# Optimization experiments

Hardware: AMD Instinct MI355X
Metric: run time of the kernel (lower is better)

## Reference

```python
import jax, jax.numpy as jnp
import numpy as np

NUM_NEURONS = 10000
D = 784
BATCH = 4096


def setup_inputs() -> dict:
    key = jax.random.key(0)
    kx, kw = jax.random.split(key)
    x = jax.random.normal(kx, (BATCH, D), dtype=jnp.float32)
    weights = jax.random.normal(kw, (NUM_NEURONS, D), dtype=jnp.float32)
    return {"x": x, "weights": weights}


def reference(x, weights):
    # SOM BMU lookup: squared distances between each input row and every
    # codebook row, argmin over the codebook, gather the winning neuron.
    # Use |a|^2 + |b|^2 - 2ab to avoid the (B, N, D) broadcast intermediate.
    x = x.reshape(-1, D)  # (B, D)
    x_sq = jnp.sum(x * x, axis=1, keepdims=True)          # (B, 1)
    w_sq = jnp.sum(weights * weights, axis=1)             # (N,)
    cross = x @ weights.T                                 # (B, N) GEMM
    distances = x_sq + w_sq[None, :] - 2.0 * cross        # (B, N)
    bmu_indices = jnp.argmin(distances, axis=1)           # (B,)
    bmu = jnp.take(weights, bmu_indices, axis=0)          # (B, D)
    return bmu
```

## Files before the change

### kernel.cpp

```cpp
#include <hip/hip_runtime.h>
#include <math.h>

#define BATCH 4096
#define D 784
#define N 10000

#define KP 800
#define NPAD 10112
#define NCHUNK 79
#define BM 128
#define BN 128
#define BK 32
#define KPL 40
#define MARGIN 3.0f

typedef __attribute__((ext_vector_type(8))) short bh8;
typedef __attribute__((ext_vector_type(4))) float fx4;

static __device__ __forceinline__ unsigned short f2bf(float f) {
    unsigned u = __float_as_uint(f);
    unsigned r = u + 0x7fffu + ((u >> 16) & 1u);
    return (unsigned short)(r >> 16);
}

static __device__ __forceinline__ void top2_insert(float w, int j, float& v0, int& i0,
                                                   float& v1, int& i1) {
    if (w < v0 || (w == v0 && j < i0)) { v1 = v0; i1 = i0; v0 = w; i0 = j; }
    else if (w < v1 || (w == v1 && j < i1)) { v1 = w; i1 = j; }
}

__global__ __launch_bounds__(256) void convert_x_kernel(const float* __restrict__ x,
                                                        unsigned short* __restrict__ xh) {
    int row = blockIdx.x;
    const float4* xr = (const float4*)(x + (size_t)row * D);
    unsigned short* dst = xh + (size_t)row * KP;
    for (int i = threadIdx.x; i < KP / 4; i += 256) {
        int k = i * 4;
        uint2 o;
        if (k < D) {
            float4 v = xr[i];
            o.x = (unsigned)f2bf(v.x) | ((unsigned)f2bf(v.y) << 16);
            o.y = (unsigned)f2bf(v.z) | ((unsigned)f2bf(v.w) << 16);
        } else { o.x = 0u; o.y = 0u; }
        *(uint2*)(dst + k) = o;
    }
}

__global__ __launch_bounds__(256) void convert_w_kernel(const float* __restrict__ w,
                                                        unsigned short* __restrict__ wh,
                                                        float* __restrict__ wsq) {
    int row = blockIdx.x;
    unsigned short* dst = wh + (size_t)row * KP;
    float s = 0.f;
    if (row < N) {
        const float4* wr = (const float4*)(w + (size_t)row * D);
        for (int i = threadIdx.x; i < KP / 4; i += 256) {
            int k = i * 4;
            uint2 o;
            if (k < D) {
                float4 v = wr[i];
                s += v.x * v.x + v.y * v.y + v.z * v.z + v.w * v.w;
                o.x = (unsigned)f2bf(v.x) | ((unsigned)f2bf(v.y) << 16);
                o.y = (unsigned)f2bf(v.z) | ((unsigned)f2bf(v.w) << 16);
            } else { o.x = 0u; o.y = 0u; }
            *(uint2*)(dst + k) = o;
        }
    } else {
        for (int i = threadIdx.x; i < KP / 4; i += 256) {
            uint2 o; o.x = 0u; o.y = 0u;
            *(uint2*)(dst + i * 4) = o;
        }
    }
    __shared__ float sred[4];
    #pragma unroll
    for (int off = 32; off; off >>= 1) s += __shfl_down(s, off);
    if ((threadIdx.x & 63) == 0) sred[threadIdx.x >> 6] = s;
    __syncthreads();
    if (threadIdx.x == 0) {
        float t = sred[0] + sred[1] + sred[2] + sred[3];
        wsq[row] = (row < N) ? t : INFINITY;
    }
}

__global__ __launch_bounds__(256) void dist_mfma_kernel(
    const unsigned short* __restrict__ xh, const unsigned short* __restrict__ wh,
    const float* __restrict__ wsq, float4* __restrict__ partial) {
    __shared__ __align__(16) unsigned short as_[BM][KPL];
    __shared__ __align__(16) unsigned short bs_[BN][KPL];
    __shared__ float4 red[BM][2];

    int tid = threadIdx.x;
    int lane = tid & 63;
    int wid = tid >> 6;
    int waveM = (wid >> 1) * 64;
    int waveN = (wid & 1) * 64;
    int rowBase = blockIdx.y * BM;
    int colBase = blockIdx.x * BN;

    fx4 acc[4][4];
    #pragma unroll
    for (int m = 0; m < 4; m++)
        #pragma unroll
        for (int n = 0; n < 4; n++) acc[m][n] = (fx4)0.f;

    int lrow = tid >> 1;
    int lseg = tid & 1;
    const unsigned short* xsrc = xh + (size_t)(rowBase + lrow) * KP + lseg * 16;
    const unsigned short* wsrc = wh + (size_t)(colBase + lrow) * KP + lseg * 16;

    for (int k0 = 0; k0 < KP; k0 += BK) {
        uint4 xa = *(const uint4*)(xsrc + k0);
        uint4 xb = *(const uint4*)(xsrc + k0 + 8);
        uint4 wa = *(const uint4*)(wsrc + k0);
        uint4 wb = *(const uint4*)(wsrc + k0 + 8);
        __syncthreads();
        *(uint4*)&as_[lrow][lseg * 16]     = xa;
        *(uint4*)&as_[lrow][lseg * 16 + 8] = xb;
        *(uint4*)&bs_[lrow][lseg * 16]     = wa;
        *(uint4*)&bs_[lrow][lseg * 16 + 8] = wb;
        __syncthreads();

        bh8 af[4], bf[4];
        #pragma unroll
        for (int m = 0; m < 4; m++)
            af[m] = *(const bh8*)&as_[waveM + m * 16 + (lane & 15)][(lane >> 4) * 8];
        #pragma unroll
        for (int n = 0; n < 4; n++)
            bf[n] = *(const bh8*)&bs_[waveN + n * 16 + (lane & 15)][(lane >> 4) * 8];
        #pragma unroll
        for (int m = 0; m < 4; m++)
            #pragma unroll
            for (int n = 0; n < 4; n++)
                acc[m][n] = __builtin_amdgcn_mfma_f32_16x16x32_bf16(af[m], bf[n],
                                                                    acc[m][n], 0, 0, 0);
    }

    float wq[4];
    #pragma unroll
    for (int n = 0; n < 4; n++)
        wq[n] = wsq[colBase + waveN + n * 16 + (lane & 15)];

    int h = lane >> 4;
    #pragma unroll
    for (int m = 0; m < 4; m++) {
        #pragma unroll
        for (int r = 0; r < 4; r++) {
            int row_local = waveM + m * 16 + h * 4 + r;
            float v0 = INFINITY, v1 = INFINITY;
            int i0 = 0x7fffffff, i1 = 0x7fffffff;
            #pragma unroll
            for (int n = 0; n < 4; n++) {
                float dv = wq[n] - 2.f * acc[m][n][r];
                int ci = colBase + waveN + n * 16 + (lane & 15);
                top2_insert(dv, ci, v0, i0, v1, i1);
            }
            #pragma unroll
            for (int mask = 1; mask < 16; mask <<= 1) {
                float w0 = __shfl_xor(v0, mask); int j0 = __shfl_xor(i0, mask);
                float w1 = __shfl_xor(v1, mask); int j1 = __shfl_xor(i1, mask);
                top2_insert(w0, j0, v0, i0, v1, i1);
                top2_insert(w1, j1, v0, i0, v1, i1);
            }
            if ((lane & 15) == 0)
                red[row_local][wid & 1] =
                    make_float4(v0, __int_as_float(i0), v1, __int_as_float(i1));
        }
    }
    __syncthreads();
    if (tid < BM) {
        float4 pa = red[tid][0], pb = red[tid][1];
        float v0 = pa.x, v1 = pa.z;
        int i0 = __float_as_int(pa.y), i1 = __float_as_int(pa.w);
        top2_insert(pb.x, __float_as_int(pb.y), v0, i0, v1, i1);
        top2_insert(pb.z, __float_as_int(pb.w), v0, i0, v1, i1);
        partial[(size_t)(rowBase + tid) * NCHUNK + blockIdx.x] =
            make_float4(v0, __int_as_float(i0), v1, __int_as_float(i1));
    }
}

__global__ __launch_bounds__(256) void rescore_kernel(const float* __restrict__ x,
                                                      const float* __restrict__ w,
                                                      const float4* __restrict__ partial,
                                                      float* __restrict__ out) {
    int wid = threadIdx.x >> 6, lane = threadIdx.x & 63;
    int row = blockIdx.x * 4 + wid;
    __shared__ int s_cnt[4];
    __shared__ int s_cand[4][64];

    const float4* part = partial + (size_t)row * NCHUNK;

    float bv = INFINITY;
    for (int c = lane; c < NCHUNK; c += 64) bv = fminf(bv, part[c].x);
    #pragma unroll
    for (int mask = 1; mask < 64; mask <<= 1) bv = fminf(bv, __shfl_xor(bv, mask));
    float thr = bv + MARGIN;

    if (lane == 0) s_cnt[wid] = 0;
    __syncthreads();
    for (int c = lane; c < NCHUNK; c += 64) {
        float4 p = part[c];
        if (p.x <= thr) {
            int pos = atomicAdd(&s_cnt[wid], 1);
            if (pos < 64) s_cand[wid][pos] = __float_as_int(p.y);
        }
        if (p.z <= thr) {
            int pos = atomicAdd(&s_cnt[wid], 1);
            if (pos < 64) s_cand[wid][pos] = __float_as_int(p.w);
        }
    }
    __syncthreads();
    int cnt = s_cnt[wid]; if (cnt > 64) cnt = 64;

    double bd = INFINITY; int bi = 0x7fffffff;
    for (int c = 0; c < cnt; c++) {
        int idx = s_cand[wid][c];
        const float* wr = w + (size_t)idx * D;
        const float* xr = x + (size_t)row * D;
        double s = 0.0;
        for (int d = lane; d < D; d += 64) {
            double wv = (double)wr[d];
            s += wv * (wv - 2.0 * (double)xr[d]);
        }
        #pragma unroll
        for (int mask = 1; mask < 64; mask <<= 1) s += __shfl_xor(s, mask);
        if (s < bd || (s == bd && idx < bi)) { bd = s; bi = idx; }
    }

    const float4* src = (const float4*)(w + (size_t)bi * D);
    float4* dst = (float4*)(out + (size_t)row * D);
    for (int i = lane; i < D / 4; i += 64) dst[i] = src[i];
}

#define FTM 64
#define FTN 128
#define FKC 16
#define FNCHUNK ((N + FTN - 1) / FTN)

__global__ __launch_bounds__(256) void wsq_kernel(const float* __restrict__ w,
                                                  float* __restrict__ wsq) {
    int row = blockIdx.x * 4 + (threadIdx.x >> 6);
    int lane = threadIdx.x & 63;
    if (row >= N) return;
    const float4* wr4 = (const float4*)(w + (size_t)row * D);
    float s = 0.f;
    for (int i = lane; i < D / 4; i += 64) {
        float4 v = wr4[i];
        s += v.x * v.x + v.y * v.y + v.z * v.z + v.w * v.w;
    }
    #pragma unroll
    for (int off = 32; off; off >>= 1) s += __shfl_down(s, off);
    if (lane == 0) wsq[row] = s;
}

__global__ __launch_bounds__(256) void dist_argmin_kernel(
    const float* __restrict__ x, const float* __restrict__ w,
    const float* __restrict__ wsq, float2* __restrict__ partial) {
    __shared__ float xs[FKC][68];
    __shared__ float wsh[FKC][132];
    int tid = threadIdx.x;
    int rowBase = blockIdx.y * FTM;
    int colBase = blockIdx.x * FTN;
    int tr = tid >> 4, tc = tid & 15;
    float acc[4][8];
    #pragma unroll
    for (int i = 0; i < 4; i++)
        #pragma unroll
        for (int j = 0; j < 8; j++) acc[i][j] = 0.f;
    int xrow = tid >> 2, xseg = tid & 3;
    for (int k0 = 0; k0 < D; k0 += FKC) {
        float4 xv = *(const float4*)&x[(size_t)(rowBase + xrow) * D + k0 + xseg * 4];
        int c0 = colBase + xrow, c1 = colBase + xrow + 64;
        float4 wv0 = (c0 < N) ? *(const float4*)&w[(size_t)c0 * D + k0 + xseg * 4]
                              : make_float4(0.f, 0.f, 0.f, 0.f);
        float4 wv1 = (c1 < N) ? *(const float4*)&w[(size_t)c1 * D + k0 + xseg * 4]
                              : make_float4(0.f, 0.f, 0.f, 0.f);
        __syncthreads();
        xs[xseg * 4 + 0][xrow] = xv.x; xs[xseg * 4 + 1][xrow] = xv.y;
        xs[xseg * 4 + 2][xrow] = xv.z; xs[xseg * 4 + 3][xrow] = xv.w;
        wsh[xseg * 4 + 0][xrow] = wv0.x; wsh[xseg * 4 + 1][xrow] = wv0.y;
        wsh[xseg * 4 + 2][xrow] = wv0.z; wsh[xseg * 4 + 3][xrow] = wv0.w;
        wsh[xseg * 4 + 0][xrow + 64] = wv1.x; wsh[xseg * 4 + 1][xrow + 64] = wv1.y;
        wsh[xseg * 4 + 2][xrow + 64] = wv1.z; wsh[xseg * 4 + 3][xrow + 64] = wv1.w;
        __syncthreads();
        #pragma unroll
        for (int k = 0; k < FKC; k++) {
            float4 a = *(const float4*)&xs[k][tr * 4];
            float4 b0 = *(const float4*)&wsh[k][tc * 8];
            float4 b1 = *(const float4*)&wsh[k][tc * 8 + 4];
            float xa[4] = {a.x, a.y, a.z, a.w};
            float wb[8] = {b0.x, b0.y, b0.z, b0.w, b1.x, b1.y, b1.z, b1.w};
            #pragma unroll
            for (int i = 0; i < 4; i++)
                #pragma unroll
                for (int j = 0; j < 8; j++) acc[i][j] = fmaf(xa[i], wb[j], acc[i][j]);
        }
    }
    float bestv[4]; int besti[4];
    #pragma unroll
    for (int i = 0; i < 4; i++) { bestv[i] = INFINITY; besti[i] = 0x7fffffff; }
    #pragma unroll
    for (int j = 0; j < 8; j++) {
        int c = colBase + tc * 8 + j;
        float wqv = (c < N) ? wsq[c] : INFINITY;
        #pragma unroll
        for (int i = 0; i < 4; i++) {
            float dv = wqv - 2.f * acc[i][j];
            if (dv < bestv[i] || (dv == bestv[i] && c < besti[i])) { bestv[i] = dv; besti[i] = c; }
        }
    }
    #pragma unroll
    for (int off = 1; off < 16; off <<= 1) {
        #pragma unroll
        for (int i = 0; i < 4; i++) {
            float ov = __shfl_xor(bestv[i], off);
            int oi = __shfl_xor(besti[i], off);
            if (ov < bestv[i] || (ov == bestv[i] && oi < besti[i])) { bestv[i] = ov; besti[i] = oi; }
        }
    }
    if (tc == 0)
        #pragma unroll
        for (int i = 0; i < 4; i++)
            partial[(size_t)(rowBase + tr * 4 + i) * FNCHUNK + blockIdx.x] =
                make_float2(bestv[i], __int_as_float(besti[i]));
}

__global__ __launch_bounds__(256) void reduce_gather_kernel(
    const float2* __restrict__ partial, const float* __restrict__ w,
    float* __restrict__ out) {
    int row = blockIdx.x, tid = threadIdx.x;
    __shared__ int s_idx;
    if (tid < 64) {
        float bv2 = INFINITY; int bi2 = 0x7fffffff;
        for (int c = tid; c < FNCHUNK; c += 64) {
            float2 p = partial[(size_t)row * FNCHUNK + c];
            int pi = __float_as_int(p.y);
            if (p.x < bv2 || (p.x == bv2 && pi < bi2)) { bv2 = p.x; bi2 = pi; }
        }
        #pragma unroll
        for (int off = 32; off; off >>= 1) {
            float ov = __shfl_down(bv2, off);
            int oi = __shfl_down(bi2, off);
            if (ov < bv2 || (ov == bv2 && oi < bi2)) { bv2 = ov; bi2 = oi; }
        }
        if (tid == 0) s_idx = bi2;
    }
    __syncthreads();
    int idx = s_idx;
    const float4* src = (const float4*)&w[(size_t)idx * D];
    float4* dst = (float4*)&out[(size_t)row * D];
    for (int i = tid; i < D / 4; i += 256) dst[i] = src[i];
}

extern "C" void kernel_launch(void* const* d_in, const int* in_sizes, int n_in,
                              void* d_out, int out_size, void* d_ws, size_t ws_size,
                              hipStream_t stream) {
    const float* x = (const float*)d_in[0];
    const float* w = (const float*)d_in[1];
    float* out = (float*)d_out;

    const size_t off_xh = 0;
    const size_t off_wh = off_xh + (size_t)BATCH * KP * 2;
    const size_t off_wsq = off_wh + (size_t)NPAD * KP * 2;
    const size_t off_part = off_wsq + (size_t)NPAD * 4 + 3648;
    const size_t need = off_part + (size_t)BATCH * NCHUNK * 16;

    if (ws_size >= need) {
        unsigned short* xh = (unsigned short*)((char*)d_ws + off_xh);
        unsigned short* wh = (unsigned short*)((char*)d_ws + off_wh);
        float* wsq = (float*)((char*)d_ws + off_wsq);
        float4* partial = (float4*)((char*)d_ws + off_part);

        hipLaunchKernelGGL(convert_x_kernel, dim3(BATCH), dim3(256), 0, stream, x, xh);
        hipLaunchKernelGGL(convert_w_kernel, dim3(NPAD), dim3(256), 0, stream, w, wh, wsq);
        hipLaunchKernelGGL(dist_mfma_kernel, dim3(NCHUNK, BATCH / BM), dim3(256), 0,
                           stream, xh, wh, wsq, partial);
        hipLaunchKernelGGL(rescore_kernel, dim3(BATCH / 4), dim3(256), 0, stream,
                           x, w, partial, out);
    } else {
        float* wsq = (float*)d_ws;
        float2* partial = (float2*)((char*)d_ws + 65536);
        hipLaunchKernelGGL(wsq_kernel, dim3((N + 3) / 4), dim3(256), 0, stream, w, wsq);
        hipLaunchKernelGGL(dist_argmin_kernel, dim3(FNCHUNK, BATCH / FTM), dim3(256), 0,
                           stream, x, w, wsq, partial);
        hipLaunchKernelGGL(reduce_gather_kernel, dim3(BATCH), dim3(256), 0, stream,
                           partial, w, out);
    }
}
```

Before: 526.2 us.

## Double-buffer MFMA GEMM with direct global-to-LDS loads and multi-chunk blocks

Restructures the bf16 MFMA distance kernel. Tiles are loaded straight into double-buffered, XOR-swizzled LDS with global_load_lds, so the copy overlaps compute and there are fewer barriers per k-step. Each block now walks four column chunks and keeps running top-2 state in registers, which cuts partial outputs and cross-lane reductions. Blocks are remapped for L2 locality, and the fallback path is removed. The cost is higher register pressure from the 16-row top-2 state and a hard dependence on the workspace being large enough.

```diff
diff --git a/kernel.cpp b/kernel.cpp
--- a/kernel.cpp
+++ b/kernel.cpp
@@ -6,16 +6,20 @@
 #define N 10000
 
 #define KP 800
-#define NPAD 10112
-#define NCHUNK 79
+#define BK 32
+#define KT (KP / BK)
 #define BM 128
 #define BN 128
-#define BK 32
-#define KPL 40
+#define CPB 4
+#define GX 20
+#define NG GX
+#define NPAD (GX * CPB * BN)
 #define MARGIN 3.0f
 
 typedef __attribute__((ext_vector_type(8))) short bh8;
 typedef __attribute__((ext_vector_type(4))) float fx4;
+typedef const __attribute__((address_space(1))) void CGV;
+typedef __attribute__((address_space(3))) void LDSV;
 
 static __device__ __forceinline__ unsigned short f2bf(float f) {
     unsigned u = __float_as_uint(f);
@@ -82,88 +86,145 @@
     }
 }
 
-__global__ __launch_bounds__(256) void dist_mfma_kernel(
+__global__ __launch_bounds__(256, 2) void dist_mfma_kernel(
     const unsigned short* __restrict__ xh, const unsigned short* __restrict__ wh,
     const float* __restrict__ wsq, float4* __restrict__ partial) {
-    __shared__ __align__(16) unsigned short as_[BM][KPL];
-    __shared__ __align__(16) unsigned short bs_[BN][KPL];
+    __shared__ __align__(16) unsigned short As[2][BM * BK];
+    __shared__ __align__(16) unsigned short Bs[2][BN * BK];
     __shared__ float4 red[BM][2];
 
-    int tid = threadIdx.x;
-    int lane = tid & 63;
-    int wid = tid >> 6;
-    int waveM = (wid >> 1) * 64;
-    int waveN = (wid & 1) * 64;
-    int rowBase = blockIdx.y * BM;
-    int colBase = blockIdx.x * BN;
-
-    fx4 acc[4][4];
-    #pragma unroll
-    for (int m = 0; m < 4; m++)
-        #pragma unroll
-        for (int n = 0; n < 4; n++) acc[m][n] = (fx4)0.f;
-
-    int lrow = tid >> 1;
-    int lseg = tid & 1;
-    const unsigned short* xsrc = xh + (size_t)(rowBase + lrow) * KP + lseg * 16;
-    const unsigned short* wsrc = wh + (size_t)(colBase + lrow) * KP + lseg * 16;
-
-    for (int k0 = 0; k0 < KP; k0 += BK) {
-        uint4 xa = *(const uint4*)(xsrc + k0);
-        uint4 xb = *(const uint4*)(xsrc + k0 + 8);
-        uint4 wa = *(const uint4*)(wsrc + k0);
-        uint4 wb = *(const uint4*)(wsrc + k0 + 8);
-        __syncthreads();
-        *(uint4*)&as_[lrow][lseg * 16]     = xa;
-        *(uint4*)&as_[lrow][lseg * 16 + 8] = xb;
-        *(uint4*)&bs_[lrow][lseg * 16]     = wa;
-        *(uint4*)&bs_[lrow][lseg * 16 + 8] = wb;
-        __syncthreads();
-
-        bh8 af[4], bf[4];
-        #pragma unroll
-        for (int m = 0; m < 4; m++)
-            af[m] = *(const bh8*)&as_[waveM + m * 16 + (lane & 15)][(lane >> 4) * 8];
-        #pragma unroll
-        for (int n = 0; n < 4; n++)
-            bf[n] = *(const bh8*)&bs_[waveN + n * 16 + (lane & 15)][(lane >> 4) * 8];
+    const int tid = threadIdx.x;
+    const int lane = tid & 63;
+    const int wid = tid >> 6;
+    const int waveM = (wid >> 1) * 64;
+    const int waveN = (wid & 1) * 64;
+
+    const int L = blockIdx.x + GX * blockIdx.y;
+    const int G = (L & 7) * 80 + (L >> 3);
+    const int bx = G >> 5;
+    const int by = G & 31;
+    const int rowBase = by * BM;
+    const int colBase0 = bx * (CPB * BN);
+
+    const int rr = tid >> 2;
+    const int csw = (tid & 3) ^ ((rr >> 1) & 3);
+    const unsigned short* aSrc0 = xh + (size_t)(rowBase + rr) * KP + csw * 8;
+    const unsigned short* aSrc1 = aSrc0 + (size_t)64 * KP;
+
+    char* ldsA0 = (char*)&As[0][0] + wid * 1024;
+    char* ldsA1 = (char*)&As[1][0] + wid * 1024;
+    char* ldsB0 = (char*)&Bs[0][0] + wid * 1024;
+    char* ldsB1 = (char*)&Bs[1][0] + wid * 1024;
+
+    int offA[4], offB[4];
+    #pragma unroll
+    for (int m = 0; m < 4; m++) {
+        int r = waveM + m * 16 + (lane & 15);
+        offA[m] = r * BK + (((lane >> 4) ^ ((r >> 1) & 3)) << 3);
+    }
+    #pragma unroll
+    for (int n = 0; n < 4; n++) {
+        int r = waveN + n * 16 + (lane & 15);
+        offB[n] = r * BK + (((lane >> 4) ^ ((r >> 1) & 3)) << 3);
+    }
+
+    float V0[16], V1[16];
+    int I0[16], I1[16];
+    #pragma unroll
+    for (int q = 0; q < 16; q++) {
+        V0[q] = INFINITY; V1[q] = INFINITY;
+        I0[q] = 0x7fffffff; I1[q] = 0x7fffffff;
+    }
+
+#define STAGE(nb, k0)                                                                  \
+    do {                                                                               \
+        __builtin_amdgcn_global_load_lds((CGV*)(aSrc0 + (k0)), (LDSV*)(ldsA##nb), 16, 0, 0);        \
+        __builtin_amdgcn_global_load_lds((CGV*)(aSrc1 + (k0)), (LDSV*)(ldsA##nb + 4096), 16, 0, 0); \
+        __builtin_amdgcn_global_load_lds((CGV*)(bSrc0 + (k0)), (LDSV*)(ldsB##nb), 16, 0, 0);        \
+        __builtin_amdgcn_global_load_lds((CGV*)(bSrc1 + (k0)), (LDSV*)(ldsB##nb + 4096), 16, 0, 0); \
+    } while (0)
+
+#define COMPUTE(nb)                                                                    \
+    do {                                                                               \
+        bh8 af[4], bf[4];                                                              \
+        _Pragma("unroll")                                                              \
+        for (int m = 0; m < 4; m++) af[m] = *(const bh8*)&As[nb][offA[m]];             \
+        _Pragma("unroll")                                                              \
+        for (int n = 0; n < 4; n++) bf[n] = *(const bh8*)&Bs[nb][offB[n]];             \
+        _Pragma("unroll")                                                              \
+        for (int m = 0; m < 4; m++)                                                    \
+            _Pragma("unroll")                                                          \
+            for (int n = 0; n < 4; n++)                                                \
+                acc[m][n] = __builtin_amdgcn_mfma_f32_16x16x32_bf16(af[m], bf[n],      \
+                                                                    acc[m][n], 0, 0, 0); \
+    } while (0)
+
+#define VM0 asm volatile("s_waitcnt vmcnt(0)" ::: "memory")
+#define BARR __builtin_amdgcn_s_barrier()
+
+    #pragma unroll 1
+    for (int c = 0; c < CPB; ++c) {
+        const int colBase = colBase0 + c * BN;
+        const unsigned short* bSrc0 = wh + (size_t)(colBase + rr) * KP + csw * 8;
+        const unsigned short* bSrc1 = bSrc0 + (size_t)64 * KP;
+
+        fx4 acc[4][4];
         #pragma unroll
         for (int m = 0; m < 4; m++)
             #pragma unroll
-            for (int n = 0; n < 4; n++)
-                acc[m][n] = __builtin_amdgcn_mfma_f32_16x16x32_bf16(af[m], bf[n],
-                                                                    acc[m][n], 0, 0, 0);
-    }
-
-    float wq[4];
-    #pragma unroll
-    for (int n = 0; n < 4; n++)
-        wq[n] = wsq[colBase + waveN + n * 16 + (lane & 15)];
-
-    int h = lane >> 4;
-    #pragma unroll
-    for (int m = 0; m < 4; m++) {
+            for (int n = 0; n < 4; n++) acc[m][n] = (fx4)0.f;
+
+        STAGE(0, 0);
+        VM0; BARR;
+        #pragma unroll 1
+        for (int t = 0; t < KT - 1; t += 2) {
+            STAGE(1, (t + 1) * BK);
+            COMPUTE(0);
+            VM0; BARR;
+            STAGE(0, (t + 2) * BK);
+            COMPUTE(1);
+            VM0; BARR;
+        }
+        COMPUTE(0);
+
+        const int cb = colBase + waveN + (lane & 15);
         #pragma unroll
-        for (int r = 0; r < 4; r++) {
-            int row_local = waveM + m * 16 + h * 4 + r;
-            float v0 = INFINITY, v1 = INFINITY;
-            int i0 = 0x7fffffff, i1 = 0x7fffffff;
+        for (int n = 0; n < 4; n++) {
+            const float wq = wsq[cb + n * 16];
+            const int ci = cb + n * 16;
             #pragma unroll
-            for (int n = 0; n < 4; n++) {
-                float dv = wq[n] - 2.f * acc[m][n][r];
-                int ci = colBase + waveN + n * 16 + (lane & 15);
-                top2_insert(dv, ci, v0, i0, v1, i1);
-            }
-            #pragma unroll
-            for (int mask = 1; mask < 16; mask <<= 1) {
-                float w0 = __shfl_xor(v0, mask); int j0 = __shfl_xor(i0, mask);
-                float w1 = __shfl_xor(v1, mask); int j1 = __shfl_xor(i1, mask);
-                top2_insert(w0, j0, v0, i0, v1, i1);
-                top2_insert(w1, j1, v0, i0, v1, i1);
-            }
-            if ((lane & 15) == 0)
-                red[row_local][wid & 1] =
-                    make_float4(v0, __int_as_float(i0), v1, __int_as_float(i1));
+            for (int m = 0; m < 4; m++)
+                #pragma unroll
+                for (int r = 0; r < 4; r++) {
+                    float dv = wq - 2.f * acc[m][n][r];
+                    top2_insert(dv, ci, V0[m * 4 + r], I0[m * 4 + r],
+                                V1[m * 4 + r], I1[m * 4 + r]);
+                }
+        }
+        __syncthreads();
+    }
+
+#undef STAGE
+#undef COMPUTE
+#undef VM0
+#undef BARR
+
+    #pragma unroll
+    for (int q = 0; q < 16; q++) {
+        float v0 = V0[q], v1 = V1[q];
+        int i0 = I0[q], i1 = I1[q];
+        #pragma unroll
+        for (int mask = 1; mask < 16; mask <<= 1) {
+            float w0 = __shfl_xor(v0, mask); int j0 = __shfl_xor(i0, mask);
+            float w1 = __shfl_xor(v1, mask); int j1 = __shfl_xor(i1, mask);
+            top2_insert(w0, j0, v0, i0, v1, i1);
+            top2_insert(w1, j1, v0, i0, v1, i1);
+        }
+        if ((lane & 15) == 0) {
+            int m = q >> 2, r = q & 3;
+            int row_local = waveM + m * 16 + (lane >> 4) * 4 + r;
+            red[row_local][wid & 1] =
+                make_float4(v0, __int_as_float(i0), v1, __int_as_float(i1));
         }
     }
     __syncthreads();
@@ -173,7 +234,7 @@
         int i0 = __float_as_int(pa.y), i1 = __float_as_int(pa.w);
         top2_insert(pb.x, __float_as_int(pb.y), v0, i0, v1, i1);
         top2_insert(pb.z, __float_as_int(pb.w), v0, i0, v1, i1);
-        partial[(size_t)(rowBase + tid) * NCHUNK + blockIdx.x] =
+        partial[(size_t)(rowBase + tid) * NG + bx] =
             make_float4(v0, __int_as_float(i0), v1, __int_as_float(i1));
     }
 }
@@ -187,17 +248,17 @@
     __shared__ int s_cnt[4];
     __shared__ int s_cand[4][64];
 
-    const float4* part = partial + (size_t)row * NCHUNK;
+    const float4* part = partial + (size_t)row * NG;
 
     float bv = INFINITY;
-    for (int c = lane; c < NCHUNK; c += 64) bv = fminf(bv, part[c].x);
+    for (int c = lane; c < NG; c += 64) bv = fminf(bv, part[c].x);
     #pragma unroll
     for (int mask = 1; mask < 64; mask <<= 1) bv = fminf(bv, __shfl_xor(bv, mask));
     float thr = bv + MARGIN;
 
     if (lane == 0) s_cnt[wid] = 0;
     __syncthreads();
-    for (int c = lane; c < NCHUNK; c += 64) {
+    for (int c = lane; c < NG; c += 64) {
         float4 p = part[c];
         if (p.x <= thr) {
             int pos = atomicAdd(&s_cnt[wid], 1);
@@ -231,126 +292,6 @@
     for (int i = lane; i < D / 4; i += 64) dst[i] = src[i];
 }
 
-#define FTM 64
-#define FTN 128
-#define FKC 16
-#define FNCHUNK ((N + FTN - 1) / FTN)
-
-__global__ __launch_bounds__(256) void wsq_kernel(const float* __restrict__ w,
-                                                  float* __restrict__ wsq) {
-    int row = blockIdx.x * 4 + (threadIdx.x >> 6);
-    int lane = threadIdx.x & 63;
-    if (row >= N) return;
-    const float4* wr4 = (const float4*)(w + (size_t)row * D);
-    float s = 0.f;
-    for (int i = lane; i < D / 4; i += 64) {
-        float4 v = wr4[i];
-        s += v.x * v.x + v.y * v.y + v.z * v.z + v.w * v.w;
-    }
-    #pragma unroll
-    for (int off = 32; off; off >>= 1) s += __shfl_down(s, off);
-    if (lane == 0) wsq[row] = s;
-}
-
-__global__ __launch_bounds__(256) void dist_argmin_kernel(
-    const float* __restrict__ x, const float* __restrict__ w,
-    const float* __restrict__ wsq, float2* __restrict__ partial) {
-    __shared__ float xs[FKC][68];
-    __shared__ float wsh[FKC][132];
-    int tid = threadIdx.x;
-    int rowBase = blockIdx.y * FTM;
-    int colBase = blockIdx.x * FTN;
-    int tr = tid >> 4, tc = tid & 15;
-    float acc[4][8];
-    #pragma unroll
-    for (int i = 0; i < 4; i++)
-        #pragma unroll
-        for (int j = 0; j < 8; j++) acc[i][j] = 0.f;
-    int xrow = tid >> 2, xseg = tid & 3;
-    for (int k0 = 0; k0 < D; k0 += FKC) {
-        float4 xv = *(const float4*)&x[(size_t)(rowBase + xrow) * D + k0 + xseg * 4];
-        int c0 = colBase + xrow, c1 = colBase + xrow + 64;
-        float4 wv0 = (c0 < N) ? *(const float4*)&w[(size_t)c0 * D + k0 + xseg * 4]
-                              : make_float4(0.f, 0.f, 0.f, 0.f);
-        float4 wv1 = (c1 < N) ? *(const float4*)&w[(size_t)c1 * D + k0 + xseg * 4]
-                              : make_float4(0.f, 0.f, 0.f, 0.f);
-        __syncthreads();
-        xs[xseg * 4 + 0][xrow] = xv.x; xs[xseg * 4 + 1][xrow] = xv.y;
-        xs[xseg * 4 + 2][xrow] = xv.z; xs[xseg * 4 + 3][xrow] = xv.w;
-        wsh[xseg * 4 + 0][xrow] = wv0.x; wsh[xseg * 4 + 1][xrow] = wv0.y;
-        wsh[xseg * 4 + 2][xrow] = wv0.z; wsh[xseg * 4 + 3][xrow] = wv0.w;
-        wsh[xseg * 4 + 0][xrow + 64] = wv1.x; wsh[xseg * 4 + 1][xrow + 64] = wv1.y;
-        wsh[xseg * 4 + 2][xrow + 64] = wv1.z; wsh[xseg * 4 + 3][xrow + 64] = wv1.w;
-        __syncthreads();
-        #pragma unroll
-        for (int k = 0; k < FKC; k++) {
-            float4 a = *(const float4*)&xs[k][tr * 4];
-            float4 b0 = *(const float4*)&wsh[k][tc * 8];
-            float4 b1 = *(const float4*)&wsh[k][tc * 8 + 4];
-            float xa[4] = {a.x, a.y, a.z, a.w};
-            float wb[8] = {b0.x, b0.y, b0.z, b0.w, b1.x, b1.y, b1.z, b1.w};
-            #pragma unroll
-            for (int i = 0; i < 4; i++)
-                #pragma unroll
-                for (int j = 0; j < 8; j++) acc[i][j] = fmaf(xa[i], wb[j], acc[i][j]);
-        }
-    }
-    float bestv[4]; int besti[4];
-    #pragma unroll
-    for (int i = 0; i < 4; i++) { bestv[i] = INFINITY; besti[i] = 0x7fffffff; }
-    #pragma unroll
-    for (int j = 0; j < 8; j++) {
-        int c = colBase + tc * 8 + j;
-        float wqv = (c < N) ? wsq[c] : INFINITY;
-        #pragma unroll
-        for (int i = 0; i < 4; i++) {
-            float dv = wqv - 2.f * acc[i][j];
-            if (dv < bestv[i] || (dv == bestv[i] && c < besti[i])) { bestv[i] = dv; besti[i] = c; }
-        }
-    }
-    #pragma unroll
-    for (int off = 1; off < 16; off <<= 1) {
-        #pragma unroll
-        for (int i = 0; i < 4; i++) {
-            float ov = __shfl_xor(bestv[i], off);
-            int oi = __shfl_xor(besti[i], off);
-            if (ov < bestv[i] || (ov == bestv[i] && oi < besti[i])) { bestv[i] = ov; besti[i] = oi; }
-        }
-    }
-    if (tc == 0)
-        #pragma unroll
-        for (int i = 0; i < 4; i++)
-            partial[(size_t)(rowBase + tr * 4 + i) * FNCHUNK + blockIdx.x] =
-                make_float2(bestv[i], __int_as_float(besti[i]));
-}
-
-__global__ __launch_bounds__(256) void reduce_gather_kernel(
-    const float2* __restrict__ partial, const float* __restrict__ w,
-    float* __restrict__ out) {
-    int row = blockIdx.x, tid = threadIdx.x;
-    __shared__ int s_idx;
-    if (tid < 64) {
-        float bv2 = INFINITY; int bi2 = 0x7fffffff;
-        for (int c = tid; c < FNCHUNK; c += 64) {
-            float2 p = partial[(size_t)row * FNCHUNK + c];
-            int pi = __float_as_int(p.y);
-            if (p.x < bv2 || (p.x == bv2 && pi < bi2)) { bv2 = p.x; bi2 = pi; }
-        }
-        #pragma unroll
-        for (int off = 32; off; off >>= 1) {
-            float ov = __shfl_down(bv2, off);
-            int oi = __shfl_down(bi2, off);
-            if (ov < bv2 || (ov == bv2 && oi < bi2)) { bv2 = ov; bi2 = oi; }
-        }
-        if (tid == 0) s_idx = bi2;
-    }
-    __syncthreads();
-    int idx = s_idx;
-    const float4* src = (const float4*)&w[(size_t)idx * D];
-    float4* dst = (float4*)&out[(size_t)row * D];
-    for (int i = tid; i < D / 4; i += 256) dst[i] = src[i];
-}
-
 extern "C" void kernel_launch(void* const* d_in, const int* in_sizes, int n_in,
                               void* d_out, int out_size, void* d_ws, size_t ws_size,
                               hipStream_t stream) {
@@ -361,28 +302,17 @@
     const size_t off_xh = 0;
     const size_t off_wh = off_xh + (size_t)BATCH * KP * 2;
     const size_t off_wsq = off_wh + (size_t)NPAD * KP * 2;
-    const size_t off_part = off_wsq + (size_t)NPAD * 4 + 3648;
-    const size_t need = off_part + (size_t)BATCH * NCHUNK * 16;
-
-    if (ws_size >= need) {
-        unsigned short* xh = (unsigned short*)((char*)d_ws + off_xh);
-        unsigned short* wh = (unsigned short*)((char*)d_ws + off_wh);
-        float* wsq = (float*)((char*)d_ws + off_wsq);
-        float4* partial = (float4*)((char*)d_ws + off_part);
-
-        hipLaunchKernelGGL(convert_x_kernel, dim3(BATCH), dim3(256), 0, stream, x, xh);
-        hipLaunchKernelGGL(convert_w_kernel, dim3(NPAD), dim3(256), 0, stream, w, wh, wsq);
-        hipLaunchKernelGGL(dist_mfma_kernel, dim3(NCHUNK, BATCH / BM), dim3(256), 0,
-                           stream, xh, wh, wsq, partial);
-        hipLaunchKernelGGL(rescore_kernel, dim3(BATCH / 4), dim3(256), 0, stream,
-                           x, w, partial, out);
-    } else {
-        float* wsq = (float*)d_ws;
-        float2* partial = (float2*)((char*)d_ws + 65536);
-        hipLaunchKernelGGL(wsq_kernel, dim3((N + 3) / 4), dim3(256), 0, stream, w, wsq);
-        hipLaunchKernelGGL(dist_argmin_kernel, dim3(FNCHUNK, BATCH / FTM), dim3(256), 0,
-                           stream, x, w, wsq, partial);
-        hipLaunchKernelGGL(reduce_gather_kernel, dim3(BATCH), dim3(256), 0, stream,
-                           partial, w, out);
-    }
-}
+    const size_t off_part = off_wsq + (size_t)NPAD * 4;
+
+    unsigned short* xh = (unsigned short*)((char*)d_ws + off_xh);
+    unsigned short* wh = (unsigned short*)((char*)d_ws + off_wh);
+    float* wsq = (float*)((char*)d_ws + off_wsq);
+    float4* partial = (float4*)((char*)d_ws + off_part);
+
+    hipLaunchKernelGGL(convert_x_kernel, dim3(BATCH), dim3(256), 0, stream, x, xh);
+    hipLaunchKernelGGL(convert_w_kernel, dim3(NPAD), dim3(256), 0, stream, w, wh, wsq);
+    hipLaunchKernelGGL(dist_mfma_kernel, dim3(GX, BATCH / BM), dim3(256), 0, stream,
+                       xh, wh, wsq, partial);
+    hipLaunchKernelGGL(rescore_kernel, dim3(BATCH / 4), dim3(256), 0, stream,
+                       x, w, partial, out);
+}
```

New measurement: 472.7 us. 1.11x faster.
